# Kernel optimization log

Hardware: AMD Instinct MI355X
Metric: run time of the kernel (lower is better)

The kernel has to match this reference:

```python
import jax, jax.numpy as jnp
import numpy as np

G, S, D, H = 32, 512, 128, 8   # num_groups, group_size, embed_dim, num_heads
HD = D // H                     # head_dim = 16
FFN = 2 * D                     # GLU hidden dim (ffn_dim = embed_dim * 2)
EPS = 1e-6


def _rmsnorm(x, w):
    return x * jax.lax.rsqrt(jnp.mean(x * x, axis=-1, keepdims=True) + EPS) * w


def setup_inputs() -> dict:
    key = jax.random.key(0)
    ks = jax.random.split(key, 12)
    BM = G * S
    s = 1.0 / float(np.sqrt(D))
    w = lambda k, shp, sc: (jax.random.normal(k, shp, jnp.float32) * sc)
    return {
        "x": jax.random.normal(ks[0], (BM, D), jnp.float32),
        "pe": jax.random.normal(ks[1], (BM, D), jnp.float32),
        "coords": jax.random.randint(ks[2], (BM, 4), 0, 128, jnp.int32),
        "Wq": w(ks[3], (D, D), s), "Wk": w(ks[4], (D, D), s),
        "Wv": w(ks[5], (D, D), s), "Wg": w(ks[6], (D, D), s),
        "Wo": w(ks[7], (D, D), s),
        "ln1_w": jnp.ones((D,), jnp.float32),
        "ln2_w": jnp.ones((D,), jnp.float32),
        "W_fc1": w(ks[8], (D, FFN), s),
        "W_gate": w(ks[9], (D, FFN), s),
        "W_fc2": w(ks[10], (FFN, D), 1.0 / float(np.sqrt(FFN))),
    }


def _decay_mask(coords):
    # coords: (BM,4) int; cols 1..3 are x,y,z voxel indices
    c = coords.reshape(G, S, 4)[..., 1:4].astype(jnp.float32)          # (G,S,3)
    dist = jnp.abs(c[:, :, None, :] - c[:, None, :, :]).sum(-1)        # (G,S,S) Manhattan
    decay = jnp.log(1.0 - 2.0 ** (-5.0 - jnp.arange(H, dtype=jnp.float32)))  # (H,)
    m = jnp.exp(dist[None] * decay[:, None, None, None])               # (H,G,S,S)
    m = jnp.nan_to_num(m)
    m = m / jnp.sqrt(m.sum(-1, keepdims=True))
    return jnp.transpose(m, (1, 0, 2, 3))                              # (G,H,S,S)


def reference(x, pe, coords, Wq, Wk, Wv, Wg, Wo, ln1_w, ln2_w, W_fc1, W_gate, W_fc2):
    mask = _decay_mask(coords)                                         # (G,H,S,S)

    # --- retention block (pre-norm) ---
    residual = x
    xn = _rmsnorm(x, ln1_w).reshape(G, S, D)
    qin = xn + pe.reshape(G, S, D)

    heads = lambda t: t.reshape(G, S, H, HD).transpose(0, 2, 1, 3)     # (G,H,S,HD)
    q = heads(qin @ Wq) * (HD ** -0.5)
    k = heads(qin @ Wk)
    v = heads(xn @ Wv)
    g = xn @ Wg                                                        # (G,S,D)

    qk = jnp.einsum('ghsd,ghtd->ghst', q, k)                           # (G,H,S,S)
    attn = jax.nn.softmax(qk, axis=-1) * mask
    denom = jnp.clip(jax.lax.stop_gradient(jnp.abs(attn).sum(-1, keepdims=True)), 1.0, None)
    attn = attn / denom
    o = jnp.einsum('ghst,ghtd->ghsd', attn, v)                         # (G,H,S,HD)
    # per-head RMSNorm (no affine), as group_norm over head_dim
    o = o * jax.lax.rsqrt(jnp.mean(o * o, axis=-1, keepdims=True) + EPS)
    o = o.transpose(0, 2, 1, 3).reshape(G, S, D)
    o = jax.nn.silu(g) * o                                             # swish output gate
    o = (o @ Wo).reshape(G * S, D)
    x1 = residual + o

    # --- GLU FFN block (pre-norm) ---
    h = _rmsnorm(x1, ln2_w)
    h = jax.nn.gelu(h @ W_fc1) * (h @ W_gate)
    return x1 + h @ W_fc2
```

## Files before the change

kernel.cpp:

```cpp
#include <hip/hip_runtime.h>

#define G_ 32
#define S_ 512
#define D_ 128
#define H_ 8
#define BM_ (G_*S_)
#define EPSF 1e-6f
#define VP_ 516

typedef float f32x4  __attribute__((ext_vector_type(4)));
typedef float f32x16 __attribute__((ext_vector_type(16)));
typedef short s16x8  __attribute__((ext_vector_type(8)));

typedef unsigned int uint32;

#if __has_builtin(__builtin_amdgcn_exp2f)
#define EXP2F(x) __builtin_amdgcn_exp2f(x)
#else
#define EXP2F(x) exp2f(x)
#endif

static __device__ __forceinline__ unsigned short f2bf(float f){
  uint32 u = __float_as_uint(f);
  u = (u + 0x7fffu + ((u >> 16) & 1u)) >> 16;
  return (unsigned short)u;
}
static __device__ __forceinline__ float bf2f(unsigned short h){
  return __uint_as_float(((uint32)h) << 16);
}
static __device__ __forceinline__ float siluf(float x){
  float e = EXP2F(-x * 1.4426950408889634f);
  return x / (1.0f + e);
}
static __device__ __forceinline__ float geluf(float x){
  float y = 0.7978845608028654f * (x + 0.044715f * x * x * x);
  y = fminf(fmaxf(y, -40.0f), 40.0f);
  float e = EXP2F(y * 2.8853900817779268f);
  float th = (e - 1.0f) / (e + 1.0f);
  return 0.5f * x * (1.0f + th);
}
static __device__ __forceinline__ uint32 sad3(uint32 a, uint32 b){
#if __has_builtin(__builtin_amdgcn_sad_u8)
  return __builtin_amdgcn_sad_u8(a, b, 0u);
#else
  uint32 d; uint32 z = 0;
  asm("v_sad_u8 %0, %1, %2, %3" : "=v"(d) : "v"(a), "v"(b), "v"(z));
  return d;
#endif
}

__global__ __launch_bounds__(256) void k_wprep_all(
    const float* __restrict__ w0, const float* __restrict__ w1,
    const float* __restrict__ w2, const float* __restrict__ w3,
    const float* __restrict__ w4, const float* __restrict__ w5,
    const float* __restrict__ w6, const float* __restrict__ w7,
    unsigned short* __restrict__ o0, unsigned short* __restrict__ o1,
    unsigned short* __restrict__ o2, unsigned short* __restrict__ o3,
    unsigned short* __restrict__ o4, unsigned short* __restrict__ o5,
    unsigned short* __restrict__ o6, unsigned short* __restrict__ o7){
  const int id = blockIdx.x * 256 + threadIdx.x;
  const float* W; unsigned short* O; int Kd, Nd, lid;
  if (id < 81920){
    const int which = id >> 14;
    W = (which == 0) ? w0 : (which == 1) ? w1 : (which == 2) ? w2 : (which == 3) ? w3 : w4;
    O = (which == 0) ? o0 : (which == 1) ? o1 : (which == 2) ? o2 : (which == 3) ? o3 : o4;
    Kd = 128; Nd = 128; lid = id & 16383;
  } else if (id < 114688){ W = w5; O = o5; Kd = 128; Nd = 256; lid = id - 81920; }
  else if (id < 147456){   W = w6; O = o6; Kd = 128; Nd = 256; lid = id - 114688; }
  else if (id < 180224){   W = w7; O = o7; Kd = 256; Nd = 128; lid = id - 147456; }
  else return;
  const int n = lid / Kd, k = lid - n * Kd;
  O[lid] = f2bf(W[(size_t)k * Nd + n]);
}

__global__ __launch_bounds__(512) void k_qkvg(
    const float* __restrict__ x, const float* __restrict__ pe,
    const float* __restrict__ ln1,
    const unsigned short* __restrict__ wqt, const unsigned short* __restrict__ wkt,
    const unsigned short* __restrict__ wvt, const unsigned short* __restrict__ wgt,
    unsigned short* __restrict__ qbf, unsigned short* __restrict__ kbf,
    unsigned short* __restrict__ vbf, unsigned short* __restrict__ gbf){
  __shared__ unsigned short wt[128 * 136];
  const int which = blockIdx.y;
  const unsigned short* WT = (which == 0) ? wqt : (which == 1) ? wkt : (which == 2) ? wvt : wgt;
  unsigned short* out      = (which == 0) ? qbf : (which == 1) ? kbf : (which == 2) ? vbf : gbf;
  const float scale = (which == 0) ? 0.36067376022224085f : 1.0f;
  const int tid = threadIdx.x;
  #pragma unroll
  for (int c = 0; c < 4; ++c){
    const int id8 = c * 512 + tid;
    const int n = id8 >> 4, k8 = id8 & 15;
    *(uint4*)&wt[n * 136 + k8 * 8] = *(const uint4*)&WT[n * 128 + k8 * 8];
  }
  const int lane = tid & 63, wave = tid >> 6;
  const int lr = lane & 15, lh = lane >> 4;
  const int rowbase = blockIdx.x * 128 + wave * 16;
  const size_t xb = (size_t)(rowbase + lr) * 128 + lh * 8;
  float xv[32];
  float ss = 0.f;
  #pragma unroll
  for (int kc = 0; kc < 4; ++kc){
    const float4 a = *(const float4*)&x[xb + kc * 32];
    const float4 b = *(const float4*)&x[xb + kc * 32 + 4];
    xv[kc*8+0]=a.x; xv[kc*8+1]=a.y; xv[kc*8+2]=a.z; xv[kc*8+3]=a.w;
    xv[kc*8+4]=b.x; xv[kc*8+5]=b.y; xv[kc*8+6]=b.z; xv[kc*8+7]=b.w;
    ss += a.x*a.x + a.y*a.y + a.z*a.z + a.w*a.w;
    ss += b.x*b.x + b.y*b.y + b.z*b.z + b.w*b.w;
  }
  ss += __shfl_xor(ss, 16, 64);
  ss += __shfl_xor(ss, 32, 64);
  const float rs = rsqrtf(ss * (1.0f / 128.0f) + EPSF);
  s16x8 af[4];
  #pragma unroll
  for (int kc = 0; kc < 4; ++kc){
    const float4 w0 = *(const float4*)&ln1[kc * 32 + lh * 8];
    const float4 w1 = *(const float4*)&ln1[kc * 32 + lh * 8 + 4];
    float n0 = xv[kc*8+0]*rs*w0.x, n1 = xv[kc*8+1]*rs*w0.y;
    float n2 = xv[kc*8+2]*rs*w0.z, n3 = xv[kc*8+3]*rs*w0.w;
    float n4 = xv[kc*8+4]*rs*w1.x, n5 = xv[kc*8+5]*rs*w1.y;
    float n6 = xv[kc*8+6]*rs*w1.z, n7 = xv[kc*8+7]*rs*w1.w;
    if (which < 2){
      const float4 p0 = *(const float4*)&pe[xb + kc * 32];
      const float4 p1 = *(const float4*)&pe[xb + kc * 32 + 4];
      n0 += p0.x; n1 += p0.y; n2 += p0.z; n3 += p0.w;
      n4 += p1.x; n5 += p1.y; n6 += p1.z; n7 += p1.w;
    }
    s16x8 r;
    r[0]=(short)f2bf(n0); r[1]=(short)f2bf(n1); r[2]=(short)f2bf(n2); r[3]=(short)f2bf(n3);
    r[4]=(short)f2bf(n4); r[5]=(short)f2bf(n5); r[6]=(short)f2bf(n6); r[7]=(short)f2bf(n7);
    af[kc] = r;
  }
  __syncthreads();
  #pragma unroll
  for (int ct = 0; ct < 8; ++ct){
    f32x4 acc = (f32x4)(0.0f);
    #pragma unroll
    for (int kc = 0; kc < 4; ++kc)
      acc = __builtin_amdgcn_mfma_f32_16x16x32_bf16(af[kc],
              *(const s16x8*)&wt[(ct * 16 + lr) * 136 + kc * 32 + lh * 8], acc, 0, 0, 0);
    #pragma unroll
    for (int j = 0; j < 4; ++j){
      const int row = rowbase + lh * 4 + j;
      const int col = ct * 16 + lr;
      out[(size_t)row * 128 + col] = f2bf(acc[j] * scale);
    }
  }
}

__global__ __launch_bounds__(256, 4) void k_attn(const unsigned short* __restrict__ qb,
    const unsigned short* __restrict__ kb, const unsigned short* __restrict__ vb,
    const int* __restrict__ coords, unsigned short* __restrict__ ob){
  __shared__ unsigned short kl[S_ * 16];
  __shared__ unsigned short vlT[16 * VP_];
  __shared__ uint32 cl1[S_];
  const int bx = blockIdx.x;
  const int g = bx >> 5, head = (bx >> 2) & 7, qtile = bx & 3;
  const int tid = threadIdx.x;
  const size_t rb = (size_t)g * S_ * 128 + head * 16;
  const int lane = tid & 63, wave = tid >> 6;
  const int lq = lane & 31, half = lane >> 5;
  const int qrow = qtile * 128 + wave * 32 + lq;
  const s16x8 bq = *(const s16x8*)(qb + rb + (size_t)qrow * 128 + half * 8);
  #pragma unroll
  for (int r = tid; r < S_; r += 256){
    const uint4* ksrc = (const uint4*)(kb + rb + (size_t)r * 128);
    ((uint4*)&kl[r * 16])[0] = ksrc[0];
    ((uint4*)&kl[r * 16])[1] = ksrc[1];
    const int4 cc = ((const int4*)coords)[g * S_ + r];
    cl1[r] = (uint32)(cc.y & 127) | ((uint32)(cc.z & 127) << 8) | ((uint32)(cc.w & 127) << 16);
  }
  {
    const int r0 = tid * 2;
    const unsigned short* v0 = vb + rb + (size_t)r0 * 128;
    const uint4 a0 = ((const uint4*)v0)[0], a1 = ((const uint4*)v0)[1];
    const uint4 b0 = ((const uint4*)(v0 + 128))[0], b1 = ((const uint4*)(v0 + 128))[1];
    const unsigned short* pa0 = (const unsigned short*)&a0;
    const unsigned short* pa1 = (const unsigned short*)&a1;
    const unsigned short* pb0 = (const unsigned short*)&b0;
    const unsigned short* pb1 = (const unsigned short*)&b1;
    #pragma unroll
    for (int hd = 0; hd < 8; ++hd){
      *(uint32*)&vlT[hd * VP_ + r0] = (uint32)pa0[hd] | ((uint32)pb0[hd] << 16);
      *(uint32*)&vlT[(hd + 8) * VP_ + r0] = (uint32)pa1[hd] | ((uint32)pb1[hd] << 16);
    }
  }
  __syncthreads();
  const float decay2 = log2f(1.0f - EXP2F(-(float)(5 + head)));
  const uint32 cs = cl1[qrow];
  f32x16 accO = (f32x16)(0.0f);
  float2 zm0 = {0.f,0.f}, zm1 = {0.f,0.f}, zm2 = {0.f,0.f}, zm3 = {0.f,0.f};
  const int vrow = (lq & 15) * VP_;
  for (int tc = 0; tc < 16; ++tc){
    const s16x8 ak = *(const s16x8*)&kl[(tc * 32 + lq) * 16 + half * 8];
    const uint4 cq0 = *(const uint4*)&cl1[tc * 32 + 4 * half];
    const uint4 cq1 = *(const uint4*)&cl1[tc * 32 + 8 + 4 * half];
    const uint4 cq2 = *(const uint4*)&cl1[tc * 32 + 16 + 4 * half];
    const uint4 cq3 = *(const uint4*)&cl1[tc * 32 + 24 + 4 * half];
    const f32x16 c = __builtin_amdgcn_mfma_f32_32x32x16_bf16(ak, bq, (f32x16)(0.0f), 0, 0, 0);
    float wv[16];
    #pragma unroll
    for (int i = 0; i < 16; ++i){
      const uint4& cq = (i < 4) ? cq0 : (i < 8) ? cq1 : (i < 12) ? cq2 : cq3;
      const uint32 ct1 = (&cq.x)[i & 3];
      const uint32 dist = sad3(cs, ct1);
      const float e2 = EXP2F((float)dist * decay2);
      const float e1 = EXP2F(c[i]);
      wv[i] = e1 * e2;
      float2& zm = (i & 2) ? ((i & 1) ? zm3 : zm2) : ((i & 1) ? zm1 : zm0);
      zm.x += e1; zm.y += e2;
    }
    union { uint32 u[4]; s16x8 v; } f0, f1;
    #pragma unroll
    for (int j = 0; j < 4; ++j){
      asm("v_cvt_pk_bf16_f32 %0, %1, %2" : "=v"(f0.u[j]) : "v"(wv[2 * j]), "v"(wv[2 * j + 1]));
      asm("v_cvt_pk_bf16_f32 %0, %1, %2" : "=v"(f1.u[j]) : "v"(wv[8 + 2 * j]), "v"(wv[9 + 2 * j]));
    }
    const int vcol = tc * 32 + 4 * half;
    union { uint32 u[4]; s16x8 v; } bv0, bv1;
    *(uint2*)&bv0.u[0] = *(const uint2*)&vlT[vrow + vcol];
    *(uint2*)&bv0.u[2] = *(const uint2*)&vlT[vrow + vcol + 8];
    *(uint2*)&bv1.u[0] = *(const uint2*)&vlT[vrow + vcol + 16];
    *(uint2*)&bv1.u[2] = *(const uint2*)&vlT[vrow + vcol + 24];
    accO = __builtin_amdgcn_mfma_f32_32x32x16_bf16(f0.v, bv0.v, accO, 0, 0, 0);
    accO = __builtin_amdgcn_mfma_f32_32x32x16_bf16(f1.v, bv1.v, accO, 0, 0, 0);
  }
  float Z = (zm0.x + zm1.x) + (zm2.x + zm3.x);
  float M = (zm0.y + zm1.y) + (zm2.y + zm3.y);
  Z += __shfl_xor(Z, 32, 64);
  M += __shfl_xor(M, 32, 64);
  const float sc = Z * sqrtf(M);
  const float epsp = EPSF * sc * sc;
  const size_t qbase = (size_t)(g * S_ + qtile * 128 + wave * 32);
  #pragma unroll
  for (int i = 0; i < 16; ++i){
    const int r = (i & 3) + 8 * (i >> 2) + 4 * half;
    const float v = accO[i];
    float ss = v * v;
    ss += __shfl_xor(ss, 1, 64); ss += __shfl_xor(ss, 2, 64);
    ss += __shfl_xor(ss, 4, 64); ss += __shfl_xor(ss, 8, 64);
    const float ei = __shfl(epsp, r, 64);
    const float on = v * rsqrtf(ss * 0.0625f + ei);
    if (lq < 16)
      ob[(qbase + r) * 128 + head * 16 + lq] = f2bf(on);
  }
}

__global__ __launch_bounds__(256) void k_wo(const unsigned short* __restrict__ g,
    const unsigned short* __restrict__ o, const unsigned short* __restrict__ WT,
    const float* __restrict__ resid, float* __restrict__ outp){
  __shared__ unsigned short wt[64 * 136];
  const int y = blockIdx.y;
  const int tid = threadIdx.x;
  #pragma unroll
  for (int c = 0; c < 4; ++c){
    const int id8 = c * 256 + tid;
    const int n = id8 >> 4, k8 = id8 & 15;
    *(uint4*)&wt[n * 136 + k8 * 8] = *(const uint4*)&WT[(size_t)(y * 64 + n) * 128 + k8 * 8];
  }
  const int lane = tid & 63, wave = tid >> 6;
  const int lr = lane & 15, lh = lane >> 4;
  const int rowbase = blockIdx.x * 64 + wave * 16;
  s16x8 af[4];
  const size_t abase = (size_t)(rowbase + lr) * 128 + lh * 8;
  #pragma unroll
  for (int kc = 0; kc < 4; ++kc){
    const s16x8 gv = *(const s16x8*)(g + abase + kc * 32);
    const s16x8 ov = *(const s16x8*)(o + abase + kc * 32);
    s16x8 r;
    #pragma unroll
    for (int j = 0; j < 8; ++j)
      r[j] = (short)f2bf(siluf(bf2f((unsigned short)gv[j])) * bf2f((unsigned short)ov[j]));
    af[kc] = r;
  }
  __syncthreads();
  #pragma unroll
  for (int ct = 0; ct < 4; ++ct){
    f32x4 acc = (f32x4)(0.0f);
    #pragma unroll
    for (int kc = 0; kc < 4; ++kc)
      acc = __builtin_amdgcn_mfma_f32_16x16x32_bf16(af[kc],
              *(const s16x8*)&wt[(ct * 16 + lr) * 136 + kc * 32 + lh * 8], acc, 0, 0, 0);
    #pragma unroll
    for (int j = 0; j < 4; ++j){
      const int row = rowbase + lh * 4 + j;
      const int col = y * 64 + ct * 16 + lr;
      const size_t idx = (size_t)row * 128 + col;
      outp[idx] = acc[j] + resid[idx];
    }
  }
}

__global__ __launch_bounds__(256) void k_dual(const float* __restrict__ x1,
    const float* __restrict__ ln2,
    const unsigned short* __restrict__ W1T, const unsigned short* __restrict__ W2T,
    unsigned short* __restrict__ hh){
  __shared__ unsigned short w1l[128 * 136];
  __shared__ unsigned short w2l[128 * 136];
  const int y = blockIdx.y;
  const int tid = threadIdx.x;
  #pragma unroll
  for (int c = 0; c < 8; ++c){
    const int id8 = c * 256 + tid;
    const int n = id8 >> 4, k8 = id8 & 15;
    *(uint4*)&w1l[n * 136 + k8 * 8] = *(const uint4*)&W1T[(size_t)(y * 128 + n) * 128 + k8 * 8];
    *(uint4*)&w2l[n * 136 + k8 * 8] = *(const uint4*)&W2T[(size_t)(y * 128 + n) * 128 + k8 * 8];
  }
  const int lane = tid & 63, wave = tid >> 6;
  const int lr = lane & 15, lh = lane >> 4;
  const int rowbase = blockIdx.x * 64 + wave * 16;
  const size_t xb = (size_t)(rowbase + lr) * 128 + lh * 8;
  float xv[32];
  float ss = 0.f;
  #pragma unroll
  for (int kc = 0; kc < 4; ++kc){
    const float4 a = *(const float4*)&x1[xb + kc * 32];
    const float4 b = *(const float4*)&x1[xb + kc * 32 + 4];
    xv[kc*8+0]=a.x; xv[kc*8+1]=a.y; xv[kc*8+2]=a.z; xv[kc*8+3]=a.w;
    xv[kc*8+4]=b.x; xv[kc*8+5]=b.y; xv[kc*8+6]=b.z; xv[kc*8+7]=b.w;
    ss += a.x*a.x + a.y*a.y + a.z*a.z + a.w*a.w;
    ss += b.x*b.x + b.y*b.y + b.z*b.z + b.w*b.w;
  }
  ss += __shfl_xor(ss, 16, 64);
  ss += __shfl_xor(ss, 32, 64);
  const float rs = rsqrtf(ss * (1.0f / 128.0f) + EPSF);
  s16x8 af[4];
  #pragma unroll
  for (int kc = 0; kc < 4; ++kc){
    const float4 w0 = *(const float4*)&ln2[kc * 32 + lh * 8];
    const float4 w1 = *(const float4*)&ln2[kc * 32 + lh * 8 + 4];
    s16x8 r;
    r[0]=(short)f2bf(xv[kc*8+0]*rs*w0.x); r[1]=(short)f2bf(xv[kc*8+1]*rs*w0.y);
    r[2]=(short)f2bf(xv[kc*8+2]*rs*w0.z); r[3]=(short)f2bf(xv[kc*8+3]*rs*w0.w);
    r[4]=(short)f2bf(xv[kc*8+4]*rs*w1.x); r[5]=(short)f2bf(xv[kc*8+5]*rs*w1.y);
    r[6]=(short)f2bf(xv[kc*8+6]*rs*w1.z); r[7]=(short)f2bf(xv[kc*8+7]*rs*w1.w);
    af[kc] = r;
  }
  __syncthreads();
  #pragma unroll
  for (int ct = 0; ct < 8; ++ct){
    f32x4 a1 = (f32x4)(0.0f), a2 = (f32x4)(0.0f);
    #pragma unroll
    for (int kc = 0; kc < 4; ++kc){
      a1 = __builtin_amdgcn_mfma_f32_16x16x32_bf16(af[kc],
             *(const s16x8*)&w1l[(ct * 16 + lr) * 136 + kc * 32 + lh * 8], a1, 0, 0, 0);
      a2 = __builtin_amdgcn_mfma_f32_16x16x32_bf16(af[kc],
             *(const s16x8*)&w2l[(ct * 16 + lr) * 136 + kc * 32 + lh * 8], a2, 0, 0, 0);
    }
    #pragma unroll
    for (int j = 0; j < 4; ++j){
      const int row = rowbase + lh * 4 + j;
      const int col = y * 128 + ct * 16 + lr;
      hh[(size_t)row * 256 + col] = f2bf(geluf(a1[j]) * a2[j]);
    }
  }
}

__global__ __launch_bounds__(256) void k_fc2(const unsigned short* __restrict__ hh,
    const unsigned short* __restrict__ WT, const float* __restrict__ x1,
    float* __restrict__ outp){
  __shared__ unsigned short wt[64 * 264];
  const int y = blockIdx.y;
  const int tid = threadIdx.x;
  #pragma unroll
  for (int c = 0; c < 8; ++c){
    const int id8 = c * 256 + tid;
    const int n = id8 >> 5, k8 = id8 & 31;
    *(uint4*)&wt[n * 264 + k8 * 8] = *(const uint4*)&WT[(size_t)(y * 64 + n) * 256 + k8 * 8];
  }
  const int lane = tid & 63, wave = tid >> 6;
  const int lr = lane & 15, lh = lane >> 4;
  const int rowbase = blockIdx.x * 64 + wave * 16;
  s16x8 af[8];
  const unsigned short* arow = hh + (size_t)(rowbase + lr) * 256 + lh * 8;
  #pragma unroll
  for (int kc = 0; kc < 8; ++kc) af[kc] = *(const s16x8*)(arow + kc * 32);
  __syncthreads();
  #pragma unroll
  for (int ct = 0; ct < 4; ++ct){
    f32x4 acc = (f32x4)(0.0f);
    #pragma unroll
    for (int kc = 0; kc < 8; ++kc)
      acc = __builtin_amdgcn_mfma_f32_16x16x32_bf16(af[kc],
              *(const s16x8*)&wt[(ct * 16 + lr) * 264 + kc * 32 + lh * 8], acc, 0, 0, 0);
    #pragma unroll
    for (int j = 0; j < 4; ++j){
      const int row = rowbase + lh * 4 + j;
      const int col = y * 64 + ct * 16 + lr;
      const size_t idx = (size_t)row * 128 + col;
      outp[idx] = acc[j] + x1[idx];
    }
  }
}

extern "C" void kernel_launch(void* const* d_in, const int* in_sizes, int n_in,
                              void* d_out, int out_size, void* d_ws, size_t ws_size,
                              hipStream_t stream){
  const float* x     = (const float*)d_in[0];
  const float* pe    = (const float*)d_in[1];
  const int*   coords= (const int*)d_in[2];
  const float* Wq    = (const float*)d_in[3];
  const float* Wk    = (const float*)d_in[4];
  const float* Wv    = (const float*)d_in[5];
  const float* Wg    = (const float*)d_in[6];
  const float* Wo    = (const float*)d_in[7];
  const float* ln1   = (const float*)d_in[8];
  const float* ln2   = (const float*)d_in[9];
  const float* Wfc1  = (const float*)d_in[10];
  const float* Wgate = (const float*)d_in[11];
  const float* Wfc2  = (const float*)d_in[12];
  float* out = (float*)d_out;
  char* ws = (char*)d_ws;

  const size_t SZB = 4194304;
  unsigned short* qbf  = (unsigned short*)(ws);
  unsigned short* kbf  = (unsigned short*)(ws + 1 * SZB);
  unsigned short* vbf  = (unsigned short*)(ws + 2 * SZB);
  unsigned short* gbf  = (unsigned short*)(ws + 3 * SZB);
  unsigned short* obf  = (unsigned short*)(ws + 4 * SZB);
  float*          x1   = (float*)(ws + 5 * SZB);
  unsigned short* hhb  = (unsigned short*)(ws + 5 * SZB + 8388608);
  char* wbase = ws + 5 * SZB + 2 * 8388608;
  unsigned short* wqt   = (unsigned short*)(wbase);
  unsigned short* wkt   = (unsigned short*)(wbase + 32768);
  unsigned short* wvt   = (unsigned short*)(wbase + 65536);
  unsigned short* wgt   = (unsigned short*)(wbase + 98304);
  unsigned short* wot   = (unsigned short*)(wbase + 131072);
  unsigned short* fc1t  = (unsigned short*)(wbase + 163840);
  unsigned short* gatet = (unsigned short*)(wbase + 229376);
  unsigned short* fc2t  = (unsigned short*)(wbase + 294912);

  dim3 b256(256);
  k_wprep_all<<<704, b256, 0, stream>>>(Wq, Wk, Wv, Wg, Wo, Wfc1, Wgate, Wfc2,
                                        wqt, wkt, wvt, wgt, wot, fc1t, gatet, fc2t);
  k_qkvg<<<dim3(128, 4), dim3(512), 0, stream>>>(x, pe, ln1, wqt, wkt, wvt, wgt,
                                                 qbf, kbf, vbf, gbf);
  k_attn<<<1024, b256, 0, stream>>>(qbf, kbf, vbf, coords, obf);
  k_wo<<<dim3(256, 2), b256, 0, stream>>>(gbf, obf, wot, x, x1);
  k_dual<<<dim3(256, 2), b256, 0, stream>>>(x1, ln2, fc1t, gatet, hhb);
  k_fc2<<<dim3(256, 2), b256, 0, stream>>>(hhb, fc2t, x1, out);
}
```

Measured before the change: 83.24 us.

## Enlarge attention blocks to 512 threads, split staging, add MFMA priority and wider stores

The attention kernel now runs 512-thread blocks that each cover 256 query rows instead of 128. This halves how often K, V and coords are staged into shared memory per group-head. Staging is divided so half the threads transpose V while the other half copy K and coords. MFMA issue is wrapped in s_setprio to favour the matrix pipe. The epilogue is reworked so every lane stores half of the rows instead of only 16 lanes storing. Risks are lower occupancy from the larger blocks, with the launch-bound min-waves setting possibly constraining registers, and fewer blocks in the grid.

```diff
diff --git a/kernel.cpp b/kernel.cpp
--- a/kernel.cpp
+++ b/kernel.cpp
@@ -147,29 +147,21 @@
   }
 }
 
-__global__ __launch_bounds__(256, 4) void k_attn(const unsigned short* __restrict__ qb,
+__global__ __launch_bounds__(512, 8) void k_attn(const unsigned short* __restrict__ qb,
     const unsigned short* __restrict__ kb, const unsigned short* __restrict__ vb,
     const int* __restrict__ coords, unsigned short* __restrict__ ob){
   __shared__ unsigned short kl[S_ * 16];
   __shared__ unsigned short vlT[16 * VP_];
   __shared__ uint32 cl1[S_];
   const int bx = blockIdx.x;
-  const int g = bx >> 5, head = (bx >> 2) & 7, qtile = bx & 3;
+  const int g = bx >> 4, head = (bx >> 1) & 7, qhalf = bx & 1;
   const int tid = threadIdx.x;
   const size_t rb = (size_t)g * S_ * 128 + head * 16;
   const int lane = tid & 63, wave = tid >> 6;
   const int lq = lane & 31, half = lane >> 5;
-  const int qrow = qtile * 128 + wave * 32 + lq;
+  const int qrow = qhalf * 256 + wave * 32 + lq;
   const s16x8 bq = *(const s16x8*)(qb + rb + (size_t)qrow * 128 + half * 8);
-  #pragma unroll
-  for (int r = tid; r < S_; r += 256){
-    const uint4* ksrc = (const uint4*)(kb + rb + (size_t)r * 128);
-    ((uint4*)&kl[r * 16])[0] = ksrc[0];
-    ((uint4*)&kl[r * 16])[1] = ksrc[1];
-    const int4 cc = ((const int4*)coords)[g * S_ + r];
-    cl1[r] = (uint32)(cc.y & 127) | ((uint32)(cc.z & 127) << 8) | ((uint32)(cc.w & 127) << 16);
-  }
-  {
+  if (tid < 256){
     const int r0 = tid * 2;
     const unsigned short* v0 = vb + rb + (size_t)r0 * 128;
     const uint4 a0 = ((const uint4*)v0)[0], a1 = ((const uint4*)v0)[1];
@@ -183,6 +175,18 @@
       *(uint32*)&vlT[hd * VP_ + r0] = (uint32)pa0[hd] | ((uint32)pb0[hd] << 16);
       *(uint32*)&vlT[(hd + 8) * VP_ + r0] = (uint32)pa1[hd] | ((uint32)pb1[hd] << 16);
     }
+  } else {
+    const int t2 = (tid - 256) * 2;
+    const uint4* k0 = (const uint4*)(kb + rb + (size_t)t2 * 128);
+    const uint4* k1 = (const uint4*)(kb + rb + (size_t)(t2 + 1) * 128);
+    ((uint4*)&kl[t2 * 16])[0] = k0[0];
+    ((uint4*)&kl[t2 * 16])[1] = k0[1];
+    ((uint4*)&kl[(t2 + 1) * 16])[0] = k1[0];
+    ((uint4*)&kl[(t2 + 1) * 16])[1] = k1[1];
+    const int4 c0 = ((const int4*)coords)[g * S_ + t2];
+    const int4 c1 = ((const int4*)coords)[g * S_ + t2 + 1];
+    cl1[t2]     = (uint32)(c0.y & 127) | ((uint32)(c0.z & 127) << 8) | ((uint32)(c0.w & 127) << 16);
+    cl1[t2 + 1] = (uint32)(c1.y & 127) | ((uint32)(c1.z & 127) << 8) | ((uint32)(c1.w & 127) << 16);
   }
   __syncthreads();
   const float decay2 = log2f(1.0f - EXP2F(-(float)(5 + head)));
@@ -196,7 +200,9 @@
     const uint4 cq1 = *(const uint4*)&cl1[tc * 32 + 8 + 4 * half];
     const uint4 cq2 = *(const uint4*)&cl1[tc * 32 + 16 + 4 * half];
     const uint4 cq3 = *(const uint4*)&cl1[tc * 32 + 24 + 4 * half];
+    __builtin_amdgcn_s_setprio(1);
     const f32x16 c = __builtin_amdgcn_mfma_f32_32x32x16_bf16(ak, bq, (f32x16)(0.0f), 0, 0, 0);
+    __builtin_amdgcn_s_setprio(0);
     float wv[16];
     #pragma unroll
     for (int i = 0; i < 16; ++i){
@@ -221,8 +227,10 @@
     *(uint2*)&bv0.u[2] = *(const uint2*)&vlT[vrow + vcol + 8];
     *(uint2*)&bv1.u[0] = *(const uint2*)&vlT[vrow + vcol + 16];
     *(uint2*)&bv1.u[2] = *(const uint2*)&vlT[vrow + vcol + 24];
+    __builtin_amdgcn_s_setprio(1);
     accO = __builtin_amdgcn_mfma_f32_32x32x16_bf16(f0.v, bv0.v, accO, 0, 0, 0);
     accO = __builtin_amdgcn_mfma_f32_32x32x16_bf16(f1.v, bv1.v, accO, 0, 0, 0);
+    __builtin_amdgcn_s_setprio(0);
   }
   float Z = (zm0.x + zm1.x) + (zm2.x + zm3.x);
   float M = (zm0.y + zm1.y) + (zm2.y + zm3.y);
@@ -230,9 +238,11 @@
   M += __shfl_xor(M, 32, 64);
   const float sc = Z * sqrtf(M);
   const float epsp = EPSF * sc * sc;
-  const size_t qbase = (size_t)(g * S_ + qtile * 128 + wave * 32);
-  #pragma unroll
-  for (int i = 0; i < 16; ++i){
+  const size_t qbase = (size_t)(g * S_ + qhalf * 256 + wave * 32);
+  const int sub = (lq >> 4);
+  #pragma unroll
+  for (int ii = 0; ii < 8; ++ii){
+    const int i = sub * 8 + ii;
     const int r = (i & 3) + 8 * (i >> 2) + 4 * half;
     const float v = accO[i];
     float ss = v * v;
@@ -240,8 +250,7 @@
     ss += __shfl_xor(ss, 4, 64); ss += __shfl_xor(ss, 8, 64);
     const float ei = __shfl(epsp, r, 64);
     const float on = v * rsqrtf(ss * 0.0625f + ei);
-    if (lq < 16)
-      ob[(qbase + r) * 128 + head * 16 + lq] = f2bf(on);
+    ob[(qbase + r) * 128 + head * 16 + (lq & 15)] = f2bf(on);
   }
 }
 
@@ -434,7 +443,7 @@
                                         wqt, wkt, wvt, wgt, wot, fc1t, gatet, fc2t);
   k_qkvg<<<dim3(128, 4), dim3(512), 0, stream>>>(x, pe, ln1, wqt, wkt, wvt, wgt,
                                                  qbf, kbf, vbf, gbf);
-  k_attn<<<1024, b256, 0, stream>>>(qbf, kbf, vbf, coords, obf);
+  k_attn<<<512, dim3(512), 0, stream>>>(qbf, kbf, vbf, coords, obf);
   k_wo<<<dim3(256, 2), b256, 0, stream>>>(gbf, obf, wot, x, x1);
   k_dual<<<dim3(256, 2), b256, 0, stream>>>(x1, ln2, fc1t, gatet, hhb);
   k_fc2<<<dim3(256, 2), b256, 0, stream>>>(hhb, fc2t, x1, out);
```

Measured after the change: 88.41 us. 1.06x slower.
